# Optimization experiments

Hardware: AMD Instinct MI355X
Metric: run time of the kernel (lower is better)

Reference implementation:

```python
import jax, jax.numpy as jnp
import numpy as np

SCALING = 2.0  # alpha / rank = 16 / 8


def _kron(A, B):
    # A: (m, n), B: (p, q) -> (m*p, n*q), same broadcast-multiply-reshape as torch code
    m, n = A.shape
    p, q = B.shape
    return (A[:, None, :, None] * B[None, :, None, :]).reshape(m * p, n * q)


def setup_inputs() -> dict:
    key = jax.random.key(0)
    k1, k2, k3, k4 = jax.random.split(key, 4)
    x = jax.random.normal(k1, (128, 8192), dtype=jnp.float32)
    original_weight = jax.random.normal(k2, (8192, 8192), dtype=jnp.float32) * 0.02
    lokr_A = jax.random.normal(k3, (512, 8192), dtype=jnp.float32) * 0.02
    lokr_B = jax.random.normal(k4, (16, 1), dtype=jnp.float32) * 0.02
    scalar = jnp.ones((1,), dtype=jnp.float32)
    return {"x": x, "original_weight": original_weight, "lokr_A": lokr_A,
            "lokr_B": lokr_B, "scalar": scalar}


def reference(x, original_weight, lokr_A, lokr_B, scalar):
    # delta_W = (A kron B) * scaling ; W_eff = W + scalar * delta_W ; out = x @ W_eff^T
    delta_W = _kron(lokr_A, lokr_B) * SCALING          # (8192, 8192)
    W_eff = original_weight + scalar[0] * delta_W      # bypass_mode with original weight
    return x @ W_eff.T                                 # dropout=0 -> identity
```

## Files before the change

kernel.cpp:

```cpp
#include <hip/hip_runtime.h>


#define M_DIM 128
#define N_DIM 8192
#define K_DIM 8192
#define BN 128
#define BK 64
#define KSPLIT 8
#define KCHUNK (K_DIM / KSPLIT)

typedef __attribute__((ext_vector_type(8))) short bf16x8;
typedef __attribute__((ext_vector_type(4))) float f32x4;

__device__ __forceinline__ unsigned short f2bf(float f) {
  unsigned u = __builtin_bit_cast(unsigned, f);
  u += 0x7FFFu + ((u >> 16) & 1u);
  return (unsigned short)(u >> 16);
}

__global__ void convert_x_kernel(const float4* __restrict__ x4,
                                 ushort4* __restrict__ xb4) {
  int t = blockIdx.x * blockDim.x + threadIdx.x;
  const int n4 = M_DIM * K_DIM / 4;
  for (int i = t; i < n4; i += gridDim.x * blockDim.x) {
    float4 v = x4[i];
    ushort4 o;
    o.x = f2bf(v.x); o.y = f2bf(v.y); o.z = f2bf(v.z); o.w = f2bf(v.w);
    xb4[i] = o;
  }
}

__global__ __launch_bounds__(256, 2) void lokr_main(
    const float* __restrict__ W,
    const float* __restrict__ A,
    const float* __restrict__ Bv,
    const float* __restrict__ scal,
    const unsigned short* __restrict__ xb,
    float* __restrict__ part)
{
  __shared__ unsigned short xs[M_DIM][BK];
  __shared__ unsigned short bs[BN + 16][BK];

  const int t    = threadIdx.x;
  const int lane = t & 63;
  const int wv   = t >> 6;
  const int bx   = blockIdx.x;
  const int ks   = bx & (KSPLIT - 1);
  const int ntb  = bx >> 3;
  const int r0   = ntb * BN;
  const int i0   = ntb * (BN / 16);
  const int kbase = ks * KCHUNK;

  const float sB = 2.0f * scal[0] * Bv[lane & 15];

  f32x4 accW[2][8];
  f32x4 accY[2];
  const f32x4 z4 = {0.f, 0.f, 0.f, 0.f};
#pragma unroll
  for (int a = 0; a < 2; ++a) {
    accY[a] = z4;
#pragma unroll
    for (int b = 0; b < 8; ++b) accW[a][b] = z4;
  }

  for (int kt = 0; kt < KCHUNK; kt += BK) {
    const int k0 = kbase + kt;
    __syncthreads();
#pragma unroll
    for (int j = 0; j < 8; ++j) {
      int c = j * 256 + t;
      int row = c >> 4, cc = c & 15;
      float4 v = *(const float4*)(W + (size_t)(r0 + row) * K_DIM + k0 + cc * 4);
      ushort4 o;
      o.x = f2bf(v.x); o.y = f2bf(v.y); o.z = f2bf(v.z); o.w = f2bf(v.w);
      *(ushort4*)&bs[row][cc * 4] = o;
    }
    {
      int row = t >> 4, cc = t & 15;
      ushort4 o;
      if (row < 8) {
        float4 v = *(const float4*)(A + (size_t)(i0 + row) * K_DIM + k0 + cc * 4);
        o.x = f2bf(v.x); o.y = f2bf(v.y); o.z = f2bf(v.z); o.w = f2bf(v.w);
      } else {
        o.x = o.y = o.z = o.w = 0;
      }
      *(ushort4*)&bs[BN + row][cc * 4] = o;
    }
#pragma unroll
    for (int j = 0; j < 4; ++j) {
      int c = j * 256 + t;
      int row = c >> 3, cc = c & 7;
      const unsigned short* g = xb + (size_t)row * K_DIM + k0 + cc * 8;
      __builtin_amdgcn_global_load_lds(
          (const __attribute__((address_space(1))) unsigned int*)g,
          (__attribute__((address_space(3))) unsigned int*)
              ((char*)&xs[0][0] + (size_t)(j * 256 + wv * 64) * 16),
          16, 0, 0);
    }
    __syncthreads();
#pragma unroll
    for (int kk = 0; kk < 2; ++kk) {
      const int koff = kk * 32 + (lane >> 4) * 8;
      bf16x8 af[2];
#pragma unroll
      for (int mt = 0; mt < 2; ++mt)
        af[mt] = *(const bf16x8*)&xs[wv * 32 + mt * 16 + (lane & 15)][koff];
#pragma unroll
      for (int n9 = 0; n9 < 9; ++n9) {
        bf16x8 bf = *(const bf16x8*)&bs[n9 * 16 + (lane & 15)][koff];
#pragma unroll
        for (int mt = 0; mt < 2; ++mt) {
          if (n9 < 8)
            accW[mt][n9] = __builtin_amdgcn_mfma_f32_16x16x32_bf16(af[mt], bf, accW[mt][n9], 0, 0, 0);
          else
            accY[mt] = __builtin_amdgcn_mfma_f32_16x16x32_bf16(af[mt], bf, accY[mt], 0, 0, 0);
        }
      }
    }
  }

  float* p = part + (size_t)ks * M_DIM * N_DIM;
#pragma unroll
  for (int mt = 0; mt < 2; ++mt) {
#pragma unroll
    for (int n9 = 0; n9 < 8; ++n9) {
      int srcl = (lane & 48) | n9;
#pragma unroll
      for (int reg = 0; reg < 4; ++reg) {
        float y2v = __shfl(accY[mt][reg], srcl, 64);
        int m = wv * 32 + mt * 16 + (lane >> 4) * 4 + reg;
        int r = r0 + n9 * 16 + (lane & 15);
        p[(size_t)m * N_DIM + r] = accW[mt][n9][reg] + sB * y2v;
      }
    }
  }
}

__global__ void reduce_kernel(const float4* __restrict__ part,
                              float4* __restrict__ out) {
  int t = blockIdx.x * blockDim.x + threadIdx.x;
  const int n4 = M_DIM * N_DIM / 4;
  for (int i = t; i < n4; i += gridDim.x * blockDim.x) {
    float4 s = part[i];
#pragma unroll
    for (int ksp = 1; ksp < KSPLIT; ++ksp) {
      float4 v = part[(size_t)ksp * n4 + i];
      s.x += v.x; s.y += v.y; s.z += v.z; s.w += v.w;
    }
    out[i] = s;
  }
}

extern "C" void kernel_launch(void* const* d_in, const int* in_sizes, int n_in,
                              void* d_out, int out_size, void* d_ws, size_t ws_size,
                              hipStream_t stream) {
  const float* x    = (const float*)d_in[0];
  const float* W    = (const float*)d_in[1];
  const float* A    = (const float*)d_in[2];
  const float* Bv   = (const float*)d_in[3];
  const float* scal = (const float*)d_in[4];
  float* out = (float*)d_out;

  unsigned short* xb = (unsigned short*)d_ws;
  float* part = (float*)((char*)d_ws + (size_t)M_DIM * K_DIM * sizeof(unsigned short));

  convert_x_kernel<<<256, 256, 0, stream>>>((const float4*)x, (ushort4*)xb);
  lokr_main<<<(N_DIM / BN) * KSPLIT, 256, 0, stream>>>(W, A, Bv, scal, xb, part);
  reduce_kernel<<<512, 256, 0, stream>>>((const float4*)part, (float4*)out);
}
```

Measured before the change: 444.9 us.

## Prefetch W/A tiles into registers and read x fragments directly from global

The W and A tiles for the next K step are now loaded into registers while the current step's MFMAs run, overlapping global latency with compute. The x tile is no longer staged in LDS; each wave reads its bf16 fragments straight from global memory (served from L2). The B tile in LDS gains padding to reduce bank conflicts. Grid sizes for the convert and reduce kernels are doubled. This adds register pressure and uncoalesced global reads for x, which may cost occupancy.

```diff
diff --git a/kernel.cpp b/kernel.cpp
--- a/kernel.cpp
+++ b/kernel.cpp
@@ -38,8 +38,7 @@
     const unsigned short* __restrict__ xb,
     float* __restrict__ part)
 {
-  __shared__ unsigned short xs[M_DIM][BK];
-  __shared__ unsigned short bs[BN + 16][BK];
+  __shared__ unsigned short bs[144][BK + 8];
 
   const int t    = threadIdx.x;
   const int lane = t & 63;
@@ -50,6 +49,7 @@
   const int r0   = ntb * BN;
   const int i0   = ntb * (BN / 16);
   const int kbase = ks * KCHUNK;
+  const int tr = t >> 4, tc = t & 15;
 
   const float sB = 2.0f * scal[0] * Bv[lane & 15];
 
@@ -63,60 +63,67 @@
     for (int b = 0; b < 8; ++b) accW[a][b] = z4;
   }
 
+  const float* Wrow = W + (size_t)(r0 + tr) * K_DIM + kbase + tc * 4;
+  const float* Arow = A + (size_t)(i0 + (tr & 7)) * K_DIM + kbase + tc * 4;
+  const bool aact = (tr < 8);
+  const unsigned short* xcol = xb + kbase;
+
+  float4 wreg[8];
+  float4 areg;
+#pragma unroll
+  for (int j = 0; j < 8; ++j)
+    wreg[j] = *(const float4*)(Wrow + (size_t)j * 16 * K_DIM);
+  if (aact) areg = *(const float4*)Arow;
+  else      { areg.x = areg.y = areg.z = areg.w = 0.f; }
+
   for (int kt = 0; kt < KCHUNK; kt += BK) {
-    const int k0 = kbase + kt;
-    __syncthreads();
 #pragma unroll
     for (int j = 0; j < 8; ++j) {
-      int c = j * 256 + t;
-      int row = c >> 4, cc = c & 15;
-      float4 v = *(const float4*)(W + (size_t)(r0 + row) * K_DIM + k0 + cc * 4);
       ushort4 o;
-      o.x = f2bf(v.x); o.y = f2bf(v.y); o.z = f2bf(v.z); o.w = f2bf(v.w);
-      *(ushort4*)&bs[row][cc * 4] = o;
+      o.x = f2bf(wreg[j].x); o.y = f2bf(wreg[j].y);
+      o.z = f2bf(wreg[j].z); o.w = f2bf(wreg[j].w);
+      *(ushort4*)&bs[j * 16 + tr][tc * 4] = o;
     }
     {
-      int row = t >> 4, cc = t & 15;
       ushort4 o;
-      if (row < 8) {
-        float4 v = *(const float4*)(A + (size_t)(i0 + row) * K_DIM + k0 + cc * 4);
-        o.x = f2bf(v.x); o.y = f2bf(v.y); o.z = f2bf(v.z); o.w = f2bf(v.w);
-      } else {
-        o.x = o.y = o.z = o.w = 0;
-      }
-      *(ushort4*)&bs[BN + row][cc * 4] = o;
-    }
-#pragma unroll
-    for (int j = 0; j < 4; ++j) {
-      int c = j * 256 + t;
-      int row = c >> 3, cc = c & 7;
-      const unsigned short* g = xb + (size_t)row * K_DIM + k0 + cc * 8;
-      __builtin_amdgcn_global_load_lds(
-          (const __attribute__((address_space(1))) unsigned int*)g,
-          (__attribute__((address_space(3))) unsigned int*)
-              ((char*)&xs[0][0] + (size_t)(j * 256 + wv * 64) * 16),
-          16, 0, 0);
+      o.x = f2bf(areg.x); o.y = f2bf(areg.y);
+      o.z = f2bf(areg.z); o.w = f2bf(areg.w);
+      *(ushort4*)&bs[128 + tr][tc * 4] = o;
     }
     __syncthreads();
+
+    if (kt + BK < KCHUNK) {
+#pragma unroll
+      for (int j = 0; j < 8; ++j)
+        wreg[j] = *(const float4*)(Wrow + (size_t)j * 16 * K_DIM + kt + BK);
+      if (aact) areg = *(const float4*)(Arow + kt + BK);
+    }
+
+    bf16x8 af[2][2];
 #pragma unroll
     for (int kk = 0; kk < 2; ++kk) {
       const int koff = kk * 32 + (lane >> 4) * 8;
-      bf16x8 af[2];
 #pragma unroll
       for (int mt = 0; mt < 2; ++mt)
-        af[mt] = *(const bf16x8*)&xs[wv * 32 + mt * 16 + (lane & 15)][koff];
+        af[kk][mt] = *(const bf16x8*)(xcol +
+            (size_t)(wv * 32 + mt * 16 + (lane & 15)) * K_DIM + kt + koff);
+    }
+#pragma unroll
+    for (int kk = 0; kk < 2; ++kk) {
+      const int koff = kk * 32 + (lane >> 4) * 8;
 #pragma unroll
       for (int n9 = 0; n9 < 9; ++n9) {
         bf16x8 bf = *(const bf16x8*)&bs[n9 * 16 + (lane & 15)][koff];
 #pragma unroll
         for (int mt = 0; mt < 2; ++mt) {
           if (n9 < 8)
-            accW[mt][n9] = __builtin_amdgcn_mfma_f32_16x16x32_bf16(af[mt], bf, accW[mt][n9], 0, 0, 0);
+            accW[mt][n9] = __builtin_amdgcn_mfma_f32_16x16x32_bf16(af[kk][mt], bf, accW[mt][n9], 0, 0, 0);
           else
-            accY[mt] = __builtin_amdgcn_mfma_f32_16x16x32_bf16(af[mt], bf, accY[mt], 0, 0, 0);
+            accY[mt] = __builtin_amdgcn_mfma_f32_16x16x32_bf16(af[kk][mt], bf, accY[mt], 0, 0, 0);
         }
       }
     }
+    __syncthreads();
   }
 
   float* p = part + (size_t)ks * M_DIM * N_DIM;
@@ -164,7 +171,7 @@
   unsigned short* xb = (unsigned short*)d_ws;
   float* part = (float*)((char*)d_ws + (size_t)M_DIM * K_DIM * sizeof(unsigned short));
 
-  convert_x_kernel<<<256, 256, 0, stream>>>((const float4*)x, (ushort4*)xb);
+  convert_x_kernel<<<512, 256, 0, stream>>>((const float4*)x, (ushort4*)xb);
   lokr_main<<<(N_DIM / BN) * KSPLIT, 256, 0, stream>>>(W, A, Bv, scal, xb, part);
-  reduce_kernel<<<512, 256, 0, stream>>>((const float4*)part, (float4*)out);
+  reduce_kernel<<<1024, 256, 0, stream>>>((const float4*)part, (float4*)out);
 }
```

Result: faster. 414.4 us (-6.9%).

## Drop LDS staging; load W/A directly into MFMA registers with pre-swizzled x

Applied to the files above, without the earlier changes.

Replaces the shared-memory tiled GEMM with a register-direct scheme. Each lane loads its own W and A row slices, converts them to bf16 and feeds them straight into 32x32x16 MFMAs, with a one-step software prefetch. The x conversion kernel now writes bf16 in MFMA fragment order so each step is a single vector load per tile. This removes the block-wide barriers and LDS traffic. The cost is strided, less coalesced global loads of W and a Y accumulation that now issues as many MFMAs as the W path.

```diff
diff --git a/kernel.cpp b/kernel.cpp
--- a/kernel.cpp
+++ b/kernel.cpp
@@ -4,13 +4,12 @@
 #define M_DIM 128
 #define N_DIM 8192
 #define K_DIM 8192
-#define BN 128
-#define BK 64
 #define KSPLIT 8
 #define KCHUNK (K_DIM / KSPLIT)
+#define STEPS (KCHUNK / 16)
 
 typedef __attribute__((ext_vector_type(8))) short bf16x8;
-typedef __attribute__((ext_vector_type(4))) float f32x4;
+typedef __attribute__((ext_vector_type(16))) float f32x16;
 
 __device__ __forceinline__ unsigned short f2bf(float f) {
   unsigned u = __builtin_bit_cast(unsigned, f);
@@ -18,16 +17,29 @@
   return (unsigned short)(u >> 16);
 }
 
-__global__ void convert_x_kernel(const float4* __restrict__ x4,
-                                 ushort4* __restrict__ xb4) {
-  int t = blockIdx.x * blockDim.x + threadIdx.x;
-  const int n4 = M_DIM * K_DIM / 4;
-  for (int i = t; i < n4; i += gridDim.x * blockDim.x) {
-    float4 v = x4[i];
-    ushort4 o;
-    o.x = f2bf(v.x); o.y = f2bf(v.y); o.z = f2bf(v.z); o.w = f2bf(v.w);
-    xb4[i] = o;
-  }
+__device__ __forceinline__ bf16x8 pack8(float4 a, float4 b) {
+  bf16x8 r;
+  r[0] = (short)f2bf(a.x); r[1] = (short)f2bf(a.y);
+  r[2] = (short)f2bf(a.z); r[3] = (short)f2bf(a.w);
+  r[4] = (short)f2bf(b.x); r[5] = (short)f2bf(b.y);
+  r[6] = (short)f2bf(b.z); r[7] = (short)f2bf(b.w);
+  return r;
+}
+
+__global__ void convert_x_kernel(const float* __restrict__ x,
+                                 unsigned short* __restrict__ xs) {
+  int tid = blockIdx.x * blockDim.x + threadIdx.x;
+  int sg   = tid >> 8;
+  int rem  = tid & 255;
+  int mt   = rem >> 6;
+  int lane = rem & 63;
+  int m  = mt * 32 + (lane & 31);
+  int kk = sg * 16 + (lane >> 5) * 8;
+  const float* src = x + (size_t)m * K_DIM + kk;
+  float4 a = *(const float4*)src;
+  float4 b = *(const float4*)(src + 4);
+  bf16x8 o = pack8(a, b);
+  *(bf16x8*)(xs + (size_t)tid * 8) = o;
 }
 
 __global__ __launch_bounds__(256, 2) void lokr_main(
@@ -35,103 +47,72 @@
     const float* __restrict__ A,
     const float* __restrict__ Bv,
     const float* __restrict__ scal,
-    const unsigned short* __restrict__ xb,
+    const unsigned short* __restrict__ xs,
     float* __restrict__ part)
 {
-  __shared__ unsigned short xs[M_DIM][BK];
-  __shared__ unsigned short bs[BN + 16][BK];
-
   const int t    = threadIdx.x;
   const int lane = t & 63;
   const int wv   = t >> 6;
   const int bx   = blockIdx.x;
   const int ks   = bx & (KSPLIT - 1);
   const int ntb  = bx >> 3;
-  const int r0   = ntb * BN;
-  const int i0   = ntb * (BN / 16);
+  const int r0   = ntb * 128;
   const int kbase = ks * KCHUNK;
+  const int l31  = lane & 31;
+  const int khalf = (lane >> 5) * 8;
 
+  const int wrow = r0 + wv * 32 + l31;
+  const int ia   = (r0 >> 4) + 2 * wv + (l31 >> 4);
   const float sB = 2.0f * scal[0] * Bv[lane & 15];
 
-  f32x4 accW[2][8];
-  f32x4 accY[2];
-  const f32x4 z4 = {0.f, 0.f, 0.f, 0.f};
+  const float* Wp = W + (size_t)wrow * K_DIM + kbase + khalf;
+  const float* Ap = A + (size_t)ia  * K_DIM + kbase + khalf;
+  const unsigned short* Xp = xs + (size_t)(ks * STEPS) * 2048 + (size_t)lane * 8;
+
+  f32x16 accW[4], accY[4];
 #pragma unroll
-  for (int a = 0; a < 2; ++a) {
-    accY[a] = z4;
+  for (int mt = 0; mt < 4; ++mt) {
 #pragma unroll
-    for (int b = 0; b < 8; ++b) accW[a][b] = z4;
+    for (int e = 0; e < 16; ++e) { accW[mt][e] = 0.f; accY[mt][e] = 0.f; }
   }
 
-  for (int kt = 0; kt < KCHUNK; kt += BK) {
-    const int k0 = kbase + kt;
-    __syncthreads();
+  float4 wc0 = *(const float4*)Wp;
+  float4 wc1 = *(const float4*)(Wp + 4);
+  float4 ac0 = *(const float4*)Ap;
+  float4 ac1 = *(const float4*)(Ap + 4);
+
+  for (int s = 0; s < STEPS; ++s) {
+    const int sn = (s + 1) & (STEPS - 1);
+    float4 wn0 = *(const float4*)(Wp + sn * 16);
+    float4 wn1 = *(const float4*)(Wp + sn * 16 + 4);
+    float4 an0 = *(const float4*)(Ap + sn * 16);
+    float4 an1 = *(const float4*)(Ap + sn * 16 + 4);
+
+    bf16x8 xf[4];
 #pragma unroll
-    for (int j = 0; j < 8; ++j) {
-      int c = j * 256 + t;
-      int row = c >> 4, cc = c & 15;
-      float4 v = *(const float4*)(W + (size_t)(r0 + row) * K_DIM + k0 + cc * 4);
-      ushort4 o;
-      o.x = f2bf(v.x); o.y = f2bf(v.y); o.z = f2bf(v.z); o.w = f2bf(v.w);
-      *(ushort4*)&bs[row][cc * 4] = o;
-    }
-    {
-      int row = t >> 4, cc = t & 15;
-      ushort4 o;
-      if (row < 8) {
-        float4 v = *(const float4*)(A + (size_t)(i0 + row) * K_DIM + k0 + cc * 4);
-        o.x = f2bf(v.x); o.y = f2bf(v.y); o.z = f2bf(v.z); o.w = f2bf(v.w);
-      } else {
-        o.x = o.y = o.z = o.w = 0;
-      }
-      *(ushort4*)&bs[BN + row][cc * 4] = o;
-    }
+    for (int mt = 0; mt < 4; ++mt)
+      xf[mt] = *(const bf16x8*)(Xp + (size_t)s * 2048 + mt * 512);
+
+    bf16x8 bw = pack8(wc0, wc1);
+    bf16x8 ba = pack8(ac0, ac1);
+
 #pragma unroll
-    for (int j = 0; j < 4; ++j) {
-      int c = j * 256 + t;
-      int row = c >> 3, cc = c & 7;
-      const unsigned short* g = xb + (size_t)row * K_DIM + k0 + cc * 8;
-      __builtin_amdgcn_global_load_lds(
-          (const __attribute__((address_space(1))) unsigned int*)g,
-          (__attribute__((address_space(3))) unsigned int*)
-              ((char*)&xs[0][0] + (size_t)(j * 256 + wv * 64) * 16),
-          16, 0, 0);
-    }
-    __syncthreads();
+    for (int mt = 0; mt < 4; ++mt)
+      accW[mt] = __builtin_amdgcn_mfma_f32_32x32x16_bf16(xf[mt], bw, accW[mt], 0, 0, 0);
 #pragma unroll
-    for (int kk = 0; kk < 2; ++kk) {
-      const int koff = kk * 32 + (lane >> 4) * 8;
-      bf16x8 af[2];
-#pragma unroll
-      for (int mt = 0; mt < 2; ++mt)
-        af[mt] = *(const bf16x8*)&xs[wv * 32 + mt * 16 + (lane & 15)][koff];
-#pragma unroll
-      for (int n9 = 0; n9 < 9; ++n9) {
-        bf16x8 bf = *(const bf16x8*)&bs[n9 * 16 + (lane & 15)][koff];
-#pragma unroll
-        for (int mt = 0; mt < 2; ++mt) {
-          if (n9 < 8)
-            accW[mt][n9] = __builtin_amdgcn_mfma_f32_16x16x32_bf16(af[mt], bf, accW[mt][n9], 0, 0, 0);
-          else
-            accY[mt] = __builtin_amdgcn_mfma_f32_16x16x32_bf16(af[mt], bf, accY[mt], 0, 0, 0);
-        }
-      }
-    }
+    for (int mt = 0; mt < 4; ++mt)
+      accY[mt] = __builtin_amdgcn_mfma_f32_32x32x16_bf16(xf[mt], ba, accY[mt], 0, 0, 0);
+
+    wc0 = wn0; wc1 = wn1; ac0 = an0; ac1 = an1;
   }
 
-  float* p = part + (size_t)ks * M_DIM * N_DIM;
+  float* p = part + (size_t)ks * M_DIM * N_DIM + r0 + wv * 32 + l31;
 #pragma unroll
-  for (int mt = 0; mt < 2; ++mt) {
+  for (int mt = 0; mt < 4; ++mt) {
 #pragma unroll
-    for (int n9 = 0; n9 < 8; ++n9) {
-      int srcl = (lane & 48) | n9;
-#pragma unroll
-      for (int reg = 0; reg < 4; ++reg) {
-        float y2v = __shfl(accY[mt][reg], srcl, 64);
-        int m = wv * 32 + mt * 16 + (lane >> 4) * 4 + reg;
-        int r = r0 + n9 * 16 + (lane & 15);
-        p[(size_t)m * N_DIM + r] = accW[mt][n9][reg] + sB * y2v;
-      }
+    for (int reg = 0; reg < 16; ++reg) {
+      int m = mt * 32 + (reg & 3) + 8 * (reg >> 2) + 4 * (lane >> 5);
+      p[(size_t)m * N_DIM] = accW[mt][reg] + sB * accY[mt][reg];
     }
   }
 }
@@ -161,10 +142,10 @@
   const float* scal = (const float*)d_in[4];
   float* out = (float*)d_out;
 
-  unsigned short* xb = (unsigned short*)d_ws;
+  unsigned short* xs = (unsigned short*)d_ws;
   float* part = (float*)((char*)d_ws + (size_t)M_DIM * K_DIM * sizeof(unsigned short));
 
-  convert_x_kernel<<<256, 256, 0, stream>>>((const float4*)x, (ushort4*)xb);
-  lokr_main<<<(N_DIM / BN) * KSPLIT, 256, 0, stream>>>(W, A, Bv, scal, xb, part);
-  reduce_kernel<<<512, 256, 0, stream>>>((const float4*)part, (float4*)out);
+  convert_x_kernel<<<512, 256, 0, stream>>>(x, xs);
+  lokr_main<<<(N_DIM / 128) * KSPLIT, 256, 0, stream>>>(W, A, Bv, scal, xs, part);
+  reduce_kernel<<<1024, 256, 0, stream>>>((const float4*)part, (float4*)out);
 }
```

Measured after the change: 434.9 us. -2.2%, faster.
